# Kernel optimization log

Measured on AMD Instinct MI355X. Metric: run time of the kernel, lower is better.

The kernel has to match this reference:

```python
import jax, jax.numpy as jnp
import numpy as np

N_NODES = 50000
N_EDGES = 1_600_000
IN_DIM = 128
OUT_DIM = 128


def setup_inputs() -> dict:
    key = jax.random.key(0)
    k1, k2, k3, k4, k5, k6 = jax.random.split(key, 6)
    H = jax.random.normal(k1, (N_NODES, IN_DIM), dtype=jnp.float32)
    edge_src = jax.random.randint(k2, (N_EDGES,), 0, N_NODES, dtype=jnp.int32)
    edge_dst = jnp.sort(jax.random.randint(k3, (N_EDGES,), 0, N_NODES, dtype=jnp.int32))
    edge_weight = jax.random.uniform(k4, (N_EDGES,), dtype=jnp.float32)
    bound = np.sqrt(6.0 / (IN_DIM + OUT_DIM))
    W = jax.random.uniform(k5, (IN_DIM, OUT_DIM), dtype=jnp.float32, minval=-bound, maxval=bound)
    b = jax.random.normal(k6, (OUT_DIM,), dtype=jnp.float32)
    return {"H": H, "edge_src": edge_src, "edge_dst": edge_dst,
            "edge_weight": edge_weight, "W": W, "b": b}


def reference(H, edge_src, edge_dst, edge_weight, W, b):
    # A_hat @ H: gather source features, scale by edge weight, scatter-sum to dst.
    msgs = edge_weight[:, None] * jnp.take(H, edge_src, axis=0)   # [E, in_dim]
    agg = jax.ops.segment_sum(msgs, edge_dst, num_segments=N_NODES)  # [N, in_dim]
    # Dense transform + bias (no activation in original forward).
    return agg @ W + b
```

## Files before the change

kernel.cpp:

```cpp
#include <hip/hip_runtime.h>

#define IN_DIM 128
#define OUT_DIM 128

typedef __attribute__((ext_vector_type(8))) short short8v;
typedef __attribute__((ext_vector_type(4))) float float4v;
typedef __attribute__((ext_vector_type(4))) unsigned int uint4v;

__device__ __forceinline__ ushort f2bf(float f) {
    unsigned int u = __builtin_bit_cast(unsigned int, f);
    unsigned int r = (u + 0x7fffu + ((u >> 16) & 1u)) >> 16;
    return (ushort)r;
}

__device__ __forceinline__ unsigned int pk2bf(float x, float y) {
#if __has_builtin(__builtin_amdgcn_cvt_pk_bf16_f32)
    typedef __attribute__((ext_vector_type(2))) __bf16 bf2;
    bf2 r = __builtin_amdgcn_cvt_pk_bf16_f32(x, y);
    return __builtin_bit_cast(unsigned int, r);
#else
    return (unsigned int)f2bf(x) | ((unsigned int)f2bf(y) << 16);
#endif
}

__global__ __launch_bounds__(256) void prep_kernel(const float* __restrict__ W,
                                                   ushort* __restrict__ Wt) {
    int k0 = blockIdx.x * 8;
    int n = threadIdx.x & 127;
    int half = threadIdx.x >> 7;
#pragma unroll
    for (int kp = 0; kp < 2; ++kp) {
        int k = k0 + (half * 2 + kp) * 2;
        float v0 = W[k * 128 + n];
        float v1 = W[(k + 1) * 128 + n];
        *(unsigned int*)&Wt[n * 136 + k] = pk2bf(v0, v1);
    }
}

__global__ __launch_bounds__(256) void gemm_kernel(const float* __restrict__ H,
                                                   const ushort* __restrict__ Wt_g,
                                                   unsigned char* __restrict__ T8,
                                                   float* __restrict__ S, int M,
                                                   const int* __restrict__ edst,
                                                   int* __restrict__ rp,
                                                   int E, int nb_gemm) {
    __shared__ ushort Ws[128 * 136];

    const int t = threadIdx.x;

    if (blockIdx.x >= nb_gemm) {
        int n = (blockIdx.x - nb_gemm) * 256 + t;
        if (n <= M) {
            int lo = 0, hi = E;
            while (lo < hi) {
                int mid = (lo + hi) >> 1;
                if (edst[mid] < n) lo = mid + 1; else hi = mid;
            }
            rp[n] = lo;
        }
        return;
    }

    const int row0 = blockIdx.x * 64;

#pragma unroll
    for (int f = t; f < 2176; f += 256)
        ((short8v*)Ws)[f] = ((const short8v*)Wt_g)[f];

    const int w = t >> 6;
    const int l = t & 63;
    const int m16 = l & 15;
    const int kq = (l >> 4) * 8;
    const int gr = row0 + w * 16 + m16;

    float4 h[8];
    if (gr < M) {
#pragma unroll
        for (int ks = 0; ks < 4; ++ks) {
            h[ks * 2]     = *(const float4*)&H[gr * 128 + ks * 32 + kq];
            h[ks * 2 + 1] = *(const float4*)&H[gr * 128 + ks * 32 + kq + 4];
        }
    } else {
#pragma unroll
        for (int i = 0; i < 8; ++i) h[i] = make_float4(0.f, 0.f, 0.f, 0.f);
    }

    short8v bfrag[4];
#pragma unroll
    for (int ks = 0; ks < 4; ++ks) {
        uint4v u;
        u[0] = pk2bf(h[ks * 2].x, h[ks * 2].y);
        u[1] = pk2bf(h[ks * 2].z, h[ks * 2].w);
        u[2] = pk2bf(h[ks * 2 + 1].x, h[ks * 2 + 1].y);
        u[3] = pk2bf(h[ks * 2 + 1].z, h[ks * 2 + 1].w);
        bfrag[ks] = __builtin_bit_cast(short8v, u);
    }

    __syncthreads();

    float4v acc[8];
#pragma unroll
    for (int nt = 0; nt < 8; ++nt) acc[nt] = (float4v){0.f, 0.f, 0.f, 0.f};

#pragma unroll
    for (int ks = 0; ks < 4; ++ks) {
#pragma unroll
        for (int nt = 0; nt < 8; ++nt) {
            short8v afrag = *(const short8v*)&Ws[(nt * 16 + m16) * 136 + ks * 32 + kq];
            acc[nt] = __builtin_amdgcn_mfma_f32_16x16x32_bf16(afrag, bfrag[ks], acc[nt], 0, 0, 0);
        }
    }

    float mx = 0.f;
#pragma unroll
    for (int nt = 0; nt < 8; ++nt) {
#pragma unroll
        for (int k = 0; k < 4; ++k) mx = fmaxf(mx, fabsf(acc[nt][k]));
    }
    mx = fmaxf(mx, __shfl_xor(mx, 16));
    mx = fmaxf(mx, __shfl_xor(mx, 32));

    const float inv = 127.0f / fmaxf(mx, 1e-20f);

    if (gr < M) {
        const int qd = l >> 4;
        if (qd == 0) S[gr] = mx * (1.0f / 127.0f);
#pragma unroll
        for (int nt = 0; nt < 8; ++nt) {
            unsigned int p = 0;
#pragma unroll
            for (int k = 0; k < 4; ++k) {
                int qi = (int)__builtin_rintf(acc[nt][k] * inv);
                qi = qi > 127 ? 127 : (qi < -127 ? -127 : qi);
                p |= ((unsigned int)(qi + 128) & 0xffu) << (k * 8);
            }
            *(unsigned int*)&T8[gr * 128 + nt * 16 + qd * 4] = p;
        }
    }
}

__global__ __launch_bounds__(256) void scatter_kernel(const unsigned char* __restrict__ T8,
                                                      const float* __restrict__ S,
                                                      const int* __restrict__ esrc,
                                                      const float* __restrict__ ew,
                                                      const int* __restrict__ rp,
                                                      const float* __restrict__ b,
                                                      float* __restrict__ out,
                                                      int M, int ngroups) {
    const int blk = blockIdx.x;
    const int halfsel = (blk & 7) >> 2;
    const int i = ((blk >> 3) << 2) + (blk & 3);
    if (i >= ngroups) return;
    const int node = i * 4 + (threadIdx.x >> 6);
    if (node >= M) return;

    const int lane = threadIdx.x & 63;
    const int quarter = lane >> 4;
    const unsigned int colb = (unsigned int)halfsel * 64u + (lane & 15u) * 4u;

    const int s = __builtin_amdgcn_readfirstlane(rp[node]);
    const int e = __builtin_amdgcn_readfirstlane(rp[node + 1]);

    float a0 = 0.f, a1 = 0.f, a2 = 0.f, a3 = 0.f;
    float B = 0.f;

    for (int c = s; c < e; c += 64) {
        const int idx = c + lane;
        int srcl = 0;
        float wl = 0.f;
        if (idx < e) { srcl = esrc[idx]; wl = ew[idx]; }
        const float wsl = wl * S[srcl];
        int nn = e - c;
        if (nn > 64) nn = 64;

        for (int j = 0; j < nn; j += 16) {
            int sq[4];
            float ws[4];
            unsigned int vv[4];
#pragma unroll
            for (int p = 0; p < 4; ++p) {
                const int sl = j + p * 4 + quarter;
                sq[p] = __shfl(srcl, sl);
                ws[p] = __shfl(wsl, sl);
            }
#pragma unroll
            for (int p = 0; p < 4; ++p)
                vv[p] = *(const unsigned int*)(T8 + ((unsigned int)sq[p] * 128u + colb));
#pragma unroll
            for (int p = 0; p < 4; ++p) {
                const unsigned int v = vv[p];
                const float w = ws[p];
                B  += w;
                a0 = fmaf((float)(v & 0xffu), w, a0);
                a1 = fmaf((float)((v >> 8) & 0xffu), w, a1);
                a2 = fmaf((float)((v >> 16) & 0xffu), w, a2);
                a3 = fmaf((float)(v >> 24), w, a3);
            }
        }
    }

    a0 += __shfl_xor(a0, 16); a0 += __shfl_xor(a0, 32);
    a1 += __shfl_xor(a1, 16); a1 += __shfl_xor(a1, 32);
    a2 += __shfl_xor(a2, 16); a2 += __shfl_xor(a2, 32);
    a3 += __shfl_xor(a3, 16); a3 += __shfl_xor(a3, 32);
    B  += __shfl_xor(B, 16);  B  += __shfl_xor(B, 32);

    if (quarter == 0) {
        const float4 bb = *(const float4*)&b[colb];
        float4 o;
        o.x = fmaf(-128.0f, B, a0) + bb.x;
        o.y = fmaf(-128.0f, B, a1) + bb.y;
        o.z = fmaf(-128.0f, B, a2) + bb.z;
        o.w = fmaf(-128.0f, B, a3) + bb.w;
        *(float4*)&out[node * 128 + colb] = o;
    }
}

extern "C" void kernel_launch(void* const* d_in, const int* in_sizes, int n_in,
                              void* d_out, int out_size, void* d_ws, size_t ws_size,
                              hipStream_t stream) {
    const float* H    = (const float*)d_in[0];
    const int*   esrc = (const int*)d_in[1];
    const int*   edst = (const int*)d_in[2];
    const float* ew   = (const float*)d_in[3];
    const float* W    = (const float*)d_in[4];
    const float* b    = (const float*)d_in[5];
    float* out = (float*)d_out;

    const int M = in_sizes[0] / IN_DIM;
    const int E = in_sizes[1];

    unsigned char* T8 = (unsigned char*)d_ws;
    size_t off = (size_t)M * 128;
    float* S  = (float*)((char*)d_ws + off);
    off += (size_t)M * 4;
    ushort* Wt = (ushort*)((char*)d_ws + off);
    off += 128 * 136 * 2;
    int* rp = (int*)((char*)d_ws + off);

    prep_kernel<<<16, 256, 0, stream>>>(W, Wt);

    const int nb_gemm = (M + 63) / 64;
    const int nb_rp   = (M + 1 + 255) / 256;
    gemm_kernel<<<nb_gemm + nb_rp, 256, 0, stream>>>(H, Wt, T8, S, M, edst, rp, E, nb_gemm);

    const int ngroups  = (M + 3) / 4;
    const int ngroups4 = ((ngroups + 3) / 4) * 4;
    const int nblk     = 2 * ngroups4;
    scatter_kernel<<<nblk, 256, 0, stream>>>(T8, S, esrc, ew, rp, b, out, M, ngroups);
}
```

Baseline: 147.9 us.

## Split quantized feature table into column halves and use nontemporal edge loads

The int8 transformed feature table is stored as two separate 64-column arrays, so each scatter block, which handles one column half, gathers from a compact table of half the size. This is meant to improve cache locality of the random row gathers. Edge index and weight loads and output stores are also made nontemporal so streaming data does not evict the gathered table from cache. Each gathered row is now 64 bytes, so access granularity per cache line changes, and nontemporal hints may do nothing or hurt.

```diff
diff --git a/kernel.cpp b/kernel.cpp
--- a/kernel.cpp
+++ b/kernel.cpp
@@ -39,7 +39,8 @@
 
 __global__ __launch_bounds__(256) void gemm_kernel(const float* __restrict__ H,
                                                    const ushort* __restrict__ Wt_g,
-                                                   unsigned char* __restrict__ T8,
+                                                   unsigned char* __restrict__ Tlo,
+                                                   unsigned char* __restrict__ Thi,
                                                    float* __restrict__ S, int M,
                                                    const int* __restrict__ edst,
                                                    int* __restrict__ rp,
@@ -134,12 +135,17 @@
                 qi = qi > 127 ? 127 : (qi < -127 ? -127 : qi);
                 p |= ((unsigned int)(qi + 128) & 0xffu) << (k * 8);
             }
-            *(unsigned int*)&T8[gr * 128 + nt * 16 + qd * 4] = p;
-        }
-    }
-}
-
-__global__ __launch_bounds__(256) void scatter_kernel(const unsigned char* __restrict__ T8,
+            const int col = nt * 16 + qd * 4;
+            if (nt < 4)
+                *(unsigned int*)&Tlo[gr * 64 + col] = p;
+            else
+                *(unsigned int*)&Thi[gr * 64 + (col - 64)] = p;
+        }
+    }
+}
+
+__global__ __launch_bounds__(256) void scatter_kernel(const unsigned char* __restrict__ Tlo,
+                                                      const unsigned char* __restrict__ Thi,
                                                       const float* __restrict__ S,
                                                       const int* __restrict__ esrc,
                                                       const float* __restrict__ ew,
@@ -154,9 +160,11 @@
     const int node = i * 4 + (threadIdx.x >> 6);
     if (node >= M) return;
 
+    const unsigned char* __restrict__ T = halfsel ? Thi : Tlo;
+
     const int lane = threadIdx.x & 63;
     const int quarter = lane >> 4;
-    const unsigned int colb = (unsigned int)halfsel * 64u + (lane & 15u) * 4u;
+    const unsigned int colb = (lane & 15u) * 4u;
 
     const int s = __builtin_amdgcn_readfirstlane(rp[node]);
     const int e = __builtin_amdgcn_readfirstlane(rp[node + 1]);
@@ -168,7 +176,10 @@
         const int idx = c + lane;
         int srcl = 0;
         float wl = 0.f;
-        if (idx < e) { srcl = esrc[idx]; wl = ew[idx]; }
+        if (idx < e) {
+            srcl = __builtin_nontemporal_load(esrc + idx);
+            wl   = __builtin_nontemporal_load(ew + idx);
+        }
         const float wsl = wl * S[srcl];
         int nn = e - c;
         if (nn > 64) nn = 64;
@@ -185,7 +196,7 @@
             }
 #pragma unroll
             for (int p = 0; p < 4; ++p)
-                vv[p] = *(const unsigned int*)(T8 + ((unsigned int)sq[p] * 128u + colb));
+                vv[p] = *(const unsigned int*)(T + ((unsigned int)sq[p] * 64u + colb));
 #pragma unroll
             for (int p = 0; p < 4; ++p) {
                 const unsigned int v = vv[p];
@@ -206,13 +217,14 @@
     B  += __shfl_xor(B, 16);  B  += __shfl_xor(B, 32);
 
     if (quarter == 0) {
-        const float4 bb = *(const float4*)&b[colb];
-        float4 o;
-        o.x = fmaf(-128.0f, B, a0) + bb.x;
-        o.y = fmaf(-128.0f, B, a1) + bb.y;
-        o.z = fmaf(-128.0f, B, a2) + bb.z;
-        o.w = fmaf(-128.0f, B, a3) + bb.w;
-        *(float4*)&out[node * 128 + colb] = o;
+        const int outcol = halfsel * 64 + (lane & 15) * 4;
+        const float4v bb = *(const float4v*)&b[outcol];
+        float4v o;
+        o[0] = fmaf(-128.0f, B, a0) + bb[0];
+        o[1] = fmaf(-128.0f, B, a1) + bb[1];
+        o[2] = fmaf(-128.0f, B, a2) + bb[2];
+        o[3] = fmaf(-128.0f, B, a3) + bb[3];
+        __builtin_nontemporal_store(o, (float4v*)&out[node * 128 + outcol]);
     }
 }
 
@@ -230,8 +242,10 @@
     const int M = in_sizes[0] / IN_DIM;
     const int E = in_sizes[1];
 
-    unsigned char* T8 = (unsigned char*)d_ws;
-    size_t off = (size_t)M * 128;
+    unsigned char* Tlo = (unsigned char*)d_ws;
+    size_t off = (size_t)M * 64;
+    unsigned char* Thi = (unsigned char*)d_ws + off;
+    off += (size_t)M * 64;
     float* S  = (float*)((char*)d_ws + off);
     off += (size_t)M * 4;
     ushort* Wt = (ushort*)((char*)d_ws + off);
@@ -242,10 +256,10 @@
 
     const int nb_gemm = (M + 63) / 64;
     const int nb_rp   = (M + 1 + 255) / 256;
-    gemm_kernel<<<nb_gemm + nb_rp, 256, 0, stream>>>(H, Wt, T8, S, M, edst, rp, E, nb_gemm);
+    gemm_kernel<<<nb_gemm + nb_rp, 256, 0, stream>>>(H, Wt, Tlo, Thi, S, M, edst, rp, E, nb_gemm);
 
     const int ngroups  = (M + 3) / 4;
     const int ngroups4 = ((ngroups + 3) / 4) * 4;
     const int nblk     = 2 * ngroups4;
-    scatter_kernel<<<nblk, 256, 0, stream>>>(T8, S, esrc, ew, rp, b, out, M, ngroups);
-}
+    scatter_kernel<<<nblk, 256, 0, stream>>>(Tlo, Thi, S, esrc, ew, rp, b, out, M, ngroups);
+}
```

Result: slower. 154.7 us (+4.6%).
